# Kernel tuning notes

Measured on AMD Instinct MI355X. Metric: run time of the kernel, lower is better.

Reference implementation:

```python
import jax, jax.numpy as jnp
import numpy as np

LEAKY_SLOPE = 0.2
NEG_INF = -9e15
LN_EPS = 1e-5


def conv1x1(x, W, b):
    # x: [B, Cin, N, L], W: [Cout, Cin], b: [Cout] -> [B, Cout, N, L]
    return jnp.einsum('bcnl,oc->bonl', x, W) + b[None, :, None, None]


def gat_layer(h, mask, W, a, concat):
    # h: [B, L, N, Fin], mask: [N, N] bool, W: [Fin, Fout], a: [2*Fout, 1]
    Wh = h @ W                                   # [B, L, N, Fout]
    F_out = W.shape[1]
    Wh1 = Wh @ a[:F_out]                         # [B, L, N, 1]
    Wh2 = Wh @ a[F_out:]                         # [B, L, N, 1]
    e = jax.nn.leaky_relu(Wh1 + jnp.swapaxes(Wh2, -1, -2), LEAKY_SLOPE)  # [B,L,N,N]
    att = jnp.where(mask, e, NEG_INF)
    att = jax.nn.softmax(att, axis=-1)
    h_prime = att @ Wh                           # [B, L, N, Fout]
    return jax.nn.elu(h_prime) if concat else h_prime


def custom_layernorm(x):
    # normalizes over dims (1, 2) as in the torch LayerNorm (affine disabled)
    m = x.mean(axis=(1, 2), keepdims=True)
    v = x.var(axis=(1, 2), keepdims=True)
    return (x - m) / jnp.sqrt(v + LN_EPS)


def setup_inputs() -> dict:
    key = jax.random.key(0)
    ks = jax.random.split(key, 16)
    B, C, N, L = 4, 256, 1024, 12
    s = 0.06  # ~xavier scale for 256-dim fans
    return {
        'x_in': jax.random.normal(ks[0], (B, C, N, L), dtype=jnp.float32),
        'D_Graph': jax.random.randint(ks[1], (N, N), 0, 2, dtype=jnp.int32),
        'nodevec1': jax.random.normal(ks[2], (N, 6), dtype=jnp.float32),
        'nodevec2': jax.random.normal(ks[3], (6, N), dtype=jnp.float32),
        'W_mlp': jax.random.normal(ks[4], (C, 2 * C), dtype=jnp.float32) * 0.04,
        'b_mlp': jnp.zeros((C,), dtype=jnp.float32),
        'W_g0': jax.random.normal(ks[5], (C, C), dtype=jnp.float32) * s,
        'a_g0': jax.random.normal(ks[6], (2 * C, 1), dtype=jnp.float32) * s,
        'W_go': jax.random.normal(ks[7], (C, C), dtype=jnp.float32) * s,
        'a_go': jax.random.normal(ks[8], (2 * C, 1), dtype=jnp.float32) * s,
        'Wg1': jax.random.normal(ks[9], (C, C), dtype=jnp.float32) * s,
        'bg1': jnp.zeros((C,), dtype=jnp.float32),
        'Wg2': jax.random.normal(ks[10], (C, C), dtype=jnp.float32) * s,
        'bg2': jnp.zeros((C,), dtype=jnp.float32),
        'Wg3': jax.random.normal(ks[11], (C, C), dtype=jnp.float32) * s,
        'bg3': jnp.zeros((C,), dtype=jnp.float32),
        'alpha': jnp.float32(-5.0),
        'weight': jnp.ones((C, N, 1), dtype=jnp.float32),
        'bias': jnp.zeros((C, N, 1), dtype=jnp.float32),
    }


def reference(x_in, D_Graph, nodevec1, nodevec2, W_mlp, b_mlp, W_g0, a_g0,
              W_go, a_go, Wg1, bg1, Wg2, bg2, Wg3, bg3, alpha, weight, bias):
    # --- adaptive-adjacency GCN branch (support_len=1, order=1) ---
    adp = jax.nn.softmax(jax.nn.relu(nodevec1 @ nodevec2), axis=1)  # [N, N]
    x1 = jnp.einsum('bcvl,wv->bcwl', x_in, adp)
    h = jnp.concatenate([x_in, x1], axis=1)                         # [B, 2C, N, L]
    x_gcn = conv1x1(h, W_mlp, b_mlp)                                # [B, C, N, L]

    # --- dense adjacency-masked GAT branch (nheads=1, order=1) ---
    mask = D_Graph > 0
    ht = jnp.transpose(x_in, (0, 3, 2, 1))                          # [B, L, N, C]
    g = gat_layer(ht, mask, W_g0, a_g0, concat=True)
    g = jax.nn.elu(gat_layer(g, mask, W_go, a_go, concat=False))
    x_gat = jnp.transpose(g, (0, 3, 2, 1))                          # [B, C, N, L]

    # --- fuse, residual, norm, GLU, affine ---
    a_s = jax.nn.sigmoid(alpha)
    x = a_s * x_gat + (1.0 - a_s) * x_gcn + x_in
    x = custom_layernorm(x)
    g1 = conv1x1(x, Wg1, bg1)
    g2 = conv1x1(x, Wg2, bg2)
    glu_out = conv1x1(g1 * jax.nn.sigmoid(g2), Wg3, bg3)
    x = glu_out + x
    x = x * weight[None] + bias[None] + x
    x = custom_layernorm(x)
    return x
```

## Files before the change

kernel.cpp:

```cpp
#include <hip/hip_runtime.h>
#include <math.h>

#define DI __device__ __forceinline__
#define AS1 __attribute__((address_space(1)))
#define AS3 __attribute__((address_space(3)))

static constexpr int  B_ = 4, C_ = 256, N_ = 1024, L_ = 12, BL_ = 48;
static constexpr long SLAB = (long)N_ * C_;
static constexpr long TOT  = (long)BL_ * SLAB;

typedef __attribute__((ext_vector_type(8))) short bf16x8;
typedef __attribute__((ext_vector_type(4))) float f32x4;

DI float b2f(uint hw) { return __builtin_bit_cast(float, (hw & 0xffffu) << 16); }
DI ushort f2b(float f) {
    uint u = __builtin_bit_cast(uint, f);
    u += 0x7FFFu + ((u >> 16) & 1u);
    return (ushort)(u >> 16);
}

DI void gload16(const void* g, void* l) {
    __builtin_amdgcn_global_load_lds((AS1 uint*)g, (AS3 uint*)l, 16, 0, 0);
}

DI float block_sum256(float v, float* sc) {
    #pragma unroll
    for (int o = 32; o > 0; o >>= 1) v += __shfl_xor(v, o, 64);
    int wid = threadIdx.x >> 6;
    __syncthreads();
    if ((threadIdx.x & 63) == 0) sc[wid] = v;
    __syncthreads();
    return sc[0] + sc[1] + sc[2] + sc[3];
}
DI float block_max256(float v, float* sc) {
    #pragma unroll
    for (int o = 32; o > 0; o >>= 1) v = fmaxf(v, __shfl_xor(v, o, 64));
    int wid = threadIdx.x >> 6;
    __syncthreads();
    if ((threadIdx.x & 63) == 0) sc[wid] = v;
    __syncthreads();
    return fmaxf(fmaxf(sc[0], sc[1]), fmaxf(sc[2], sc[3]));
}

__global__ __launch_bounds__(256) void k_adp(const float* __restrict__ nv1,
                                             const float* __restrict__ nv2,
                                             ushort* __restrict__ adp) {
    __shared__ float r[6];
    __shared__ float sc[4];
    int row = blockIdx.x, tid = threadIdx.x;
    if (tid < 6) r[tid] = nv1[row * 6 + tid];
    __syncthreads();
    float e[4];
    #pragma unroll
    for (int q = 0; q < 4; q++) {
        int j = tid + q * 256;
        float s = 0.f;
        #pragma unroll
        for (int k = 0; k < 6; k++) s += r[k] * nv2[k * 1024 + j];
        e[q] = s > 0.f ? s : 0.f;
    }
    float m = fmaxf(fmaxf(e[0], e[1]), fmaxf(e[2], e[3]));
    m = block_max256(m, sc);
    float ps = 0.f;
    #pragma unroll
    for (int q = 0; q < 4; q++) { e[q] = __expf(e[q] - m); ps += e[q]; }
    ps = block_sum256(ps, sc);
    float rinv = 1.f / ps;
    #pragma unroll
    for (int q = 0; q < 4; q++) adp[(long)row * 1024 + tid + q * 256] = f2b(e[q] * rinv);
}

__global__ __launch_bounds__(256) void k_tin(const float* __restrict__ x,
                                             ushort* __restrict__ xb,
                                             float* __restrict__ xf) {
    __shared__ float t[64][65];
    int nl0 = blockIdx.x * 64, c0 = blockIdx.y * 64, b = blockIdx.z;
    int lx = threadIdx.x & 63, ly = threadIdx.x >> 6;
    #pragma unroll
    for (int i = 0; i < 16; i++) {
        int c = c0 + ly + i * 4;
        t[ly + i * 4][lx] = x[(long)(b * 256 + c) * 12288 + nl0 + lx];
    }
    __syncthreads();
    #pragma unroll
    for (int i = 0; i < 16; i++) {
        int nl = nl0 + ly + i * 4;
        int n = nl / 12, l = nl % 12;
        long idx = ((long)(b * 12 + l) * 1024 + n) * 256 + c0 + lx;
        float v = t[lx][ly + i * 4];
        xb[idx] = f2b(v);
        xf[idx] = v;
    }
}

__global__ __launch_bounds__(256) void k_xtt(const ushort* __restrict__ X,
                                             ushort* __restrict__ XT) {
    __shared__ ushort t[64][68];
    int bl = blockIdx.z;
    int n0 = blockIdx.x * 64, c0 = blockIdx.y * 64;
    int lx = threadIdx.x & 63, ly = threadIdx.x >> 6;
    const ushort* Xp = X + (long)bl * SLAB;
    #pragma unroll
    for (int i = 0; i < 16; i++)
        t[ly + i * 4][lx] = Xp[(long)(n0 + ly + i * 4) * 256 + c0 + lx];
    __syncthreads();
    ushort* Tp = XT + (long)bl * SLAB;
    #pragma unroll
    for (int i = 0; i < 16; i++)
        Tp[(long)(c0 + ly + i * 4) * 1024 + n0 + lx] = t[lx][ly + i * 4];
}

__global__ __launch_bounds__(256) void k_wt2(const float* __restrict__ S0, ushort* __restrict__ D0,
                                             const float* __restrict__ S1, ushort* __restrict__ D1) {
    __shared__ float t[64][65];
    const float* S = blockIdx.z ? S1 : S0;
    ushort* D = blockIdx.z ? D1 : D0;
    int c0 = blockIdx.x * 64, o0 = blockIdx.y * 64;
    int lx = threadIdx.x & 63, ly = threadIdx.x >> 6;
    #pragma unroll
    for (int i = 0; i < 16; i++)
        t[ly + i * 4][lx] = S[(long)(c0 + ly + i * 4) * 256 + o0 + lx];
    __syncthreads();
    #pragma unroll
    for (int i = 0; i < 16; i++)
        D[(long)(o0 + ly + i * 4) * 256 + c0 + lx] = f2b(t[lx][ly + i * 4]);
}

__global__ __launch_bounds__(256) void k_wconv(const float* __restrict__ S, ushort* __restrict__ D) {
    long i = (long)blockIdx.x * 256 + threadIdx.x;
    D[i] = f2b(S[i]);
}

__global__ __launch_bounds__(256) void k_wgi(const float* __restrict__ W1, const float* __restrict__ b1,
                                             const float* __restrict__ W2, const float* __restrict__ b2,
                                             ushort* __restrict__ WGI, float* __restrict__ BI) {
    int n = blockIdx.x, p = n >> 5, q = n & 31;
    const float* src = (q < 16) ? W1 + (long)(p * 16 + q) * 256
                                : W2 + (long)(p * 16 + q - 16) * 256;
    WGI[(long)n * 256 + threadIdx.x] = f2b(src[threadIdx.x]);
    if (threadIdx.x == 0) BI[n] = (q < 16) ? b1[p * 16 + q] : b2[p * 16 + q - 16];
}

__global__ __launch_bounds__(256) void k_va(const float* __restrict__ W, const float* __restrict__ a,
                                            float* __restrict__ va) {
    __shared__ float sc[4];
    int c = blockIdx.x, t = threadIdx.x;
    float w = W[(long)c * 256 + t];
    float s1 = block_sum256(w * a[t], sc);
    float s2 = block_sum256(w * a[256 + t], sc);
    if (t == 0) { va[c] = s1; va[256 + c] = s2; }
}

__global__ __launch_bounds__(256) void k_wtprep(const float* __restrict__ w,
                                                const float* __restrict__ b,
                                                float* __restrict__ wt,
                                                float* __restrict__ bt) {
    int n = blockIdx.x, c = threadIdx.x;
    wt[(long)n * 256 + c] = w[(long)c * 1024 + n] + 1.f;
    bt[(long)n * 256 + c] = b[(long)c * 1024 + n];
}

__global__ __launch_bounds__(256) void k_maskpack(const int* __restrict__ dg,
                                                  uint* __restrict__ maskw) {
    int w = blockIdx.x * 256 + threadIdx.x;
    int row = w >> 5, wo = w & 31;
    uint m = 0;
    #pragma unroll
    for (int b = 0; b < 32; b++)
        m |= (dg[(long)row * 1024 + wo * 32 + b] > 0 ? 1u : 0u) << b;
    maskw[w] = m;
}

template<int NPAIR, int GLU>
__global__ __launch_bounds__(256) void k_bgemm(
    const ushort* __restrict__ A0, long sA0,
    const ushort* __restrict__ A1, long sA1,
    int lda, int K0, int KK,
    const ushort* __restrict__ Bt, long sBt,
    const float* __restrict__ bias,
    float* __restrict__ Cf, ushort* __restrict__ Cb, long sC,
    const float* __restrict__ biasi) {
    __shared__ ushort As[128 * 32];
    __shared__ ushort Bs[128 * 32];
    const int tid = threadIdx.x;
    const int bl = blockIdx.z;
    const int m0 = blockIdx.x * 128, n0 = blockIdx.y * 128;
    const int N = gridDim.y * 128;
    const int lane = tid & 63, w = tid >> 6;
    const int wm = (w >> 1) * 64, wn = (w & 1) * 64;
    const int sr = tid >> 2, sk = (tid & 3) * 8;
    const int fr = lane & 15, fk = (lane >> 4) * 8;
    f32x4 acc[4][4] = {};
    const ushort* Ab0 = A0 + (long)bl * sA0;
    const ushort* Ab1 = (NPAIR == 2) ? A1 + (long)bl * sA1 : nullptr;
    const ushort* Bb = Bt + (long)bl * sBt;
    for (int k0 = 0; k0 < KK; k0 += 32) {
        const ushort* Asrc = Ab0; int kl = k0;
        if (NPAIR == 2 && k0 >= K0) { Asrc = Ab1; kl = k0 - K0; }
        __syncthreads();
        gload16(&Asrc[(long)(m0 + sr) * lda + kl + sk],      &As[sr * 32 + sk]);
        gload16(&Asrc[(long)(m0 + sr + 64) * lda + kl + sk], &As[(sr + 64) * 32 + sk]);
        gload16(&Bb[(long)(n0 + sr) * KK + k0 + sk],         &Bs[sr * 32 + sk]);
        gload16(&Bb[(long)(n0 + sr + 64) * KK + k0 + sk],    &Bs[(sr + 64) * 32 + sk]);
        __syncthreads();
        bf16x8 af[4], bg[4];
        #pragma unroll
        for (int i = 0; i < 4; i++) {
            af[i] = *(const bf16x8*)&As[(wm + i * 16 + fr) * 32 + fk];
            bg[i] = *(const bf16x8*)&Bs[(wn + i * 16 + fr) * 32 + fk];
        }
        #pragma unroll
        for (int i = 0; i < 4; i++)
            #pragma unroll
            for (int j = 0; j < 4; j++)
                acc[i][j] = __builtin_amdgcn_mfma_f32_16x16x32_bf16(af[i], bg[j], acc[i][j], 0, 0, 0);
    }
    const int cn = lane & 15, rb = (lane >> 4) * 4;
    if (GLU) {
        #pragma unroll
        for (int nt = 0; nt < 4; nt += 2) {
            int n1 = n0 + wn + nt * 16 + cn;
            int hcol = ((n1 >> 5) << 4) + cn;
            float b1 = biasi[n1], b2 = biasi[n1 + 16];
            #pragma unroll
            for (int i = 0; i < 4; i++) {
                #pragma unroll
                for (int r = 0; r < 4; r++) {
                    int m = m0 + wm + i * 16 + rb + r;
                    float g1 = acc[i][nt][r] + b1;
                    float g2 = acc[i][nt + 1][r] + b2;
                    float h = g1 / (1.f + __expf(-g2));
                    Cb[(long)bl * sC + (long)m * 256 + hcol] = f2b(h);
                }
            }
        }
    } else {
        #pragma unroll
        for (int j = 0; j < 4; j++) {
            int n = n0 + wn + j * 16 + cn;
            float bv = bias ? bias[n] : 0.f;
            #pragma unroll
            for (int i = 0; i < 4; i++) {
                #pragma unroll
                for (int r = 0; r < 4; r++) {
                    int m = m0 + wm + i * 16 + rb + r;
                    float v = acc[i][j][r] + bv;
                    long idx = (long)bl * sC + (long)m * N + n;
                    if (Cf) Cf[idx] = v;
                    if (Cb) Cb[idx] = f2b(v);
                }
            }
        }
    }
}

__global__ __launch_bounds__(256) void k_dots(const ushort* __restrict__ X,
                                              const float* __restrict__ va,
                                              float* __restrict__ o1,
                                              float* __restrict__ o2) {
    int wid = threadIdx.x >> 6, lane = threadIdx.x & 63;
    long row = (long)blockIdx.x * 4 + wid;
    uint2 xv = *(const uint2*)(X + row * 256 + lane * 4);
    float x0 = b2f(xv.x), x1 = b2f(xv.x >> 16), x2 = b2f(xv.y), x3 = b2f(xv.y >> 16);
    float4 v1 = *(const float4*)&va[lane * 4];
    float4 v2 = *(const float4*)&va[256 + lane * 4];
    float s1 = x0 * v1.x + x1 * v1.y + x2 * v1.z + x3 * v1.w;
    float s2 = x0 * v2.x + x1 * v2.y + x2 * v2.z + x3 * v2.w;
    #pragma unroll
    for (int o = 32; o > 0; o >>= 1) { s1 += __shfl_xor(s1, o, 64); s2 += __shfl_xor(s2, o, 64); }
    if (lane == 0) { o1[row] = s1; o2[row] = s2; }
}

DI float attn_p(float w1, float w2, uint bit, float mr) {
    float e = w1 + w2;
    e = e > 0.f ? e : 0.2f * e;
    float p = __expf(e - mr);
    return bit ? p : 0.f;
}

__global__ __launch_bounds__(256) void k_attn_mf(
    const ushort* __restrict__ WhT,
    const float* __restrict__ w1v, const float* __restrict__ w2v,
    const uint* __restrict__ maskw,
    ushort* __restrict__ outB) {
    __shared__ ushort P2[32 * 64 * 8];
    __shared__ float w2s[1024];
    __shared__ float w1s[64];
    __shared__ uint msk[64 * 33];
    __shared__ float pmax[4][64];
    __shared__ float psum[4][64];
    __shared__ float mrow[64];
    __shared__ float ssum[64];
    __shared__ float rsv[64];
    int d = blockIdx.x;
    int lidx = (d & 7) * 96 + (d >> 3);
    int bl = lidx >> 4;
    int i0 = (lidx & 15) * 64;
    int tid = threadIdx.x;
    #pragma unroll
    for (int q = 0; q < 4; q++) w2s[tid + q * 256] = w2v[(long)bl * 1024 + tid + q * 256];
    if (tid < 64) w1s[tid] = w1v[(long)bl * 1024 + i0 + tid];
    {
        const uint4* gm = (const uint4*)(maskw + (long)i0 * 32);
        uint4 ma = gm[tid * 2], mb = gm[tid * 2 + 1];
        int r0 = tid >> 2, w0 = (tid & 3) * 8;
        uint* mp = &msk[r0 * 33 + w0];
        mp[0] = ma.x; mp[1] = ma.y; mp[2] = ma.z; mp[3] = ma.w;
        mp[4] = mb.x; mp[5] = mb.y; mp[6] = mb.z; mp[7] = mb.w;
    }
    __syncthreads();
    const int row = tid & 63, jt = tid >> 6;
    float mloc = -1e30f;
    #pragma unroll
    for (int wq = 0; wq < 8; wq++) {
        uint mw = msk[row * 33 + jt * 8 + wq];
        int jb = jt * 256 + wq * 32;
        #pragma unroll
        for (int b = 0; b < 32; b++)
            mloc = fmaxf(mloc, ((mw >> b) & 1) ? w2s[jb + b] : -1e30f);
    }
    pmax[jt][row] = mloc;
    __syncthreads();
    if (tid < 64) {
        float m = fmaxf(fmaxf(pmax[0][tid], pmax[1][tid]), fmaxf(pmax[2][tid], pmax[3][tid]));
        float e = w1s[tid] + m;
        mrow[tid] = (e > 0.f) ? e : 0.2f * e;
        ssum[tid] = 0.f;
    }
    __syncthreads();
    const int lane = tid & 63, w = tid >> 6;
    const int wn = w * 64;
    const int fr = lane & 15, fk8 = (lane >> 4) * 8;
    f32x4 acc[4][4] = {};
    const ushort* bp = WhT + (long)bl * SLAB;
    const float w1r = w1s[row];
    const float mr = mrow[row];
    #pragma unroll 1
    for (int jc = 0; jc < 4; jc++) {
        int j0 = jc * 256;
        bf16x8 bgbuf[2][4];
        #pragma unroll
        for (int nt = 0; nt < 4; nt++)
            bgbuf[0][nt] = *(const bf16x8*)&bp[(long)(wn + nt * 16 + fr) * 1024 + j0 + fk8];
        uint mw0 = msk[row * 33 + jc * 8 + jt * 2];
        uint mw1 = msk[row * 33 + jc * 8 + jt * 2 + 1];
        float sloc = 0.f;
        #pragma unroll
        for (int u = 0; u < 8; u++) {
            uint mg = ((u & 4) ? mw1 : mw0) >> ((u & 3) * 8);
            int jb = j0 + jt * 64 + u * 8;
            float p0 = attn_p(w1r, w2s[jb + 0], mg & 1, mr);
            float p1 = attn_p(w1r, w2s[jb + 1], (mg >> 1) & 1, mr);
            float p2 = attn_p(w1r, w2s[jb + 2], (mg >> 2) & 1, mr);
            float p3 = attn_p(w1r, w2s[jb + 3], (mg >> 3) & 1, mr);
            float p4 = attn_p(w1r, w2s[jb + 4], (mg >> 4) & 1, mr);
            float p5 = attn_p(w1r, w2s[jb + 5], (mg >> 5) & 1, mr);
            float p6 = attn_p(w1r, w2s[jb + 6], (mg >> 6) & 1, mr);
            float p7 = attn_p(w1r, w2s[jb + 7], (mg >> 7) & 1, mr);
            sloc += p0 + p1 + p2 + p3 + p4 + p5 + p6 + p7;
            uint4 pv;
            pv.x = (uint)f2b(p0) | ((uint)f2b(p1) << 16);
            pv.y = (uint)f2b(p2) | ((uint)f2b(p3) << 16);
            pv.z = (uint)f2b(p4) | ((uint)f2b(p5) << 16);
            pv.w = (uint)f2b(p6) | ((uint)f2b(p7) << 16);
            int kq = jt * 8 + u;
            *(uint4*)((char*)P2 + (kq * 64 + row) * 16) = pv;
        }
        psum[jt][row] = sloc;
        __syncthreads();
        if (tid < 64)
            ssum[tid] += psum[0][tid] + psum[1][tid] + psum[2][tid] + psum[3][tid];
        #pragma unroll
        for (int ks = 0; ks < 8; ks++) {
            if (ks < 7) {
                int kb = (ks + 1) * 32 + fk8;
                #pragma unroll
                for (int nt = 0; nt < 4; nt++)
                    bgbuf[(ks + 1) & 1][nt] =
                        *(const bf16x8*)&bp[(long)(wn + nt * 16 + fr) * 1024 + j0 + kb];
            }
            int kq = ks * 4 + (lane >> 4);
            bf16x8 af[4];
            #pragma unroll
            for (int mt = 0; mt < 4; mt++)
                af[mt] = *(const bf16x8*)((char*)P2 + (kq * 64 + mt * 16 + fr) * 16);
            #pragma unroll
            for (int mt = 0; mt < 4; mt++)
                #pragma unroll
                for (int nt = 0; nt < 4; nt++)
                    acc[mt][nt] = __builtin_amdgcn_mfma_f32_16x16x32_bf16(
                        af[mt], bgbuf[ks & 1][nt], acc[mt][nt], 0, 0, 0);
        }
        __syncthreads();
    }
    if (tid < 64) rsv[tid] = 1.f / ssum[tid];
    __syncthreads();
    #pragma unroll
    for (int mt = 0; mt < 4; mt++) {
        #pragma unroll
        for (int r = 0; r < 4; r++) {
            int i = mt * 16 + (lane >> 4) * 4 + r;
            float sc = rsv[i];
            #pragma unroll
            for (int nt = 0; nt < 4; nt++) {
                int c = wn + nt * 16 + fr;
                float v = acc[mt][nt][r] * sc;
                v = (v > 0.f) ? v : __expf(v) - 1.f;
                outB[(long)bl * SLAB + (long)(i0 + i) * 256 + c] = f2b(v);
            }
        }
    }
}

__global__ __launch_bounds__(256) void k_fuse_ln(const ushort* __restrict__ gat,
                                                 const float4* __restrict__ gcn,
                                                 const float4* __restrict__ xf,
                                                 const float* __restrict__ alpha,
                                                 float4* __restrict__ o,
                                                 float2* __restrict__ part) {
    __shared__ float sc[4];
    int bl = blockIdx.y;
    long i = (long)bl * 65536 + blockIdx.x * 256 + threadIdx.x;
    float as = 1.f / (1.f + __expf(-alpha[0]));
    float bs = 1.f - as;
    uint2 hv = ((const uint2*)gat)[i];
    float4 g = gcn[i], x = xf[i];
    float4 v = make_float4(as * b2f(hv.x) + bs * g.x + x.x,
                           as * b2f(hv.x >> 16) + bs * g.y + x.y,
                           as * b2f(hv.y) + bs * g.z + x.z,
                           as * b2f(hv.y >> 16) + bs * g.w + x.w);
    o[i] = v;
    float s = v.x + v.y + v.z + v.w;
    float q = v.x * v.x + v.y * v.y + v.z * v.z + v.w * v.w;
    s = block_sum256(s, sc);
    q = block_sum256(q, sc);
    if (threadIdx.x == 0) part[bl * 256 + blockIdx.x] = make_float2(s, q);
}

__global__ __launch_bounds__(256) void k_stats256(const float2* __restrict__ part,
                                                  float2* __restrict__ stats) {
    __shared__ float sc[4];
    int bl = blockIdx.x;
    float2 v = part[bl * 256 + threadIdx.x];
    float s = block_sum256(v.x, sc);
    float q = block_sum256(v.y, sc);
    if (threadIdx.x == 0) {
        float mean = s / (float)SLAB;
        float var = q / (float)SLAB - mean * mean;
        stats[bl] = make_float2(mean, 1.f / sqrtf(var + 1e-5f));
    }
}

__global__ __launch_bounds__(256) void k_ln_apply(const float4* __restrict__ x,
                                                  const float2* __restrict__ stats,
                                                  float4* __restrict__ o,
                                                  ushort* __restrict__ ob) {
    long i = (long)blockIdx.x * 256 + threadIdx.x;
    int bl = (int)(i >> 16);
    float2 st = stats[bl];
    float4 v = x[i];
    float o0 = (v.x - st.x) * st.y, o1 = (v.y - st.x) * st.y;
    float o2 = (v.z - st.x) * st.y, o3 = (v.w - st.x) * st.y;
    o[i] = make_float4(o0, o1, o2, o3);
    uint2 ow;
    ow.x = (uint)f2b(o0) | ((uint)f2b(o1) << 16);
    ow.y = (uint)f2b(o2) | ((uint)f2b(o3) << 16);
    ((uint2*)ob)[i] = ow;
}

__global__ __launch_bounds__(256) void k_finpre_ln(const float4* __restrict__ glu,
                                                   const float4* __restrict__ xn,
                                                   const float4* __restrict__ wt,
                                                   const float4* __restrict__ bt,
                                                   float4* __restrict__ o,
                                                   float2* __restrict__ part) {
    __shared__ float sc[4];
    int bl = blockIdx.y;
    long i = (long)bl * 65536 + blockIdx.x * 256 + threadIdx.x;
    long wi = i & 65535;
    float4 g = glu[i], x = xn[i], w = wt[wi], b = bt[wi];
    float4 v = make_float4((g.x + x.x) * w.x + b.x, (g.y + x.y) * w.y + b.y,
                           (g.z + x.z) * w.z + b.z, (g.w + x.w) * w.w + b.w);
    o[i] = v;
    float s = v.x + v.y + v.z + v.w;
    float q = v.x * v.x + v.y * v.y + v.z * v.z + v.w * v.w;
    s = block_sum256(s, sc);
    q = block_sum256(q, sc);
    if (threadIdx.x == 0) part[bl * 256 + blockIdx.x] = make_float2(s, q);
}

__global__ __launch_bounds__(256) void k_out(const float* __restrict__ x,
                                             const float2* __restrict__ stats,
                                             float* __restrict__ out) {
    int n = blockIdx.x, b = blockIdx.y, c = threadIdx.x;
    float v[12];
    #pragma unroll
    for (int l = 0; l < 12; l++) {
        float2 st = stats[b * 12 + l];
        float t = x[(long)(b * 12 + l) * SLAB + (long)n * 256 + c];
        v[l] = (t - st.x) * st.y;
    }
    float4* op = (float4*)(out + ((long)(b * 256 + c) * 1024 + n) * 12);
    op[0] = make_float4(v[0], v[1], v[2], v[3]);
    op[1] = make_float4(v[4], v[5], v[6], v[7]);
    op[2] = make_float4(v[8], v[9], v[10], v[11]);
}

extern "C" void kernel_launch(void* const* d_in, const int* in_sizes, int n_in,
                              void* d_out, int out_size, void* d_ws, size_t ws_size,
                              hipStream_t stream) {
    (void)in_sizes; (void)n_in; (void)out_size; (void)ws_size;
    const float* x_in = (const float*)d_in[0];
    const int*   dg   = (const int*)d_in[1];
    const float* nv1  = (const float*)d_in[2];
    const float* nv2  = (const float*)d_in[3];
    const float* Wmlp = (const float*)d_in[4];
    const float* bmlp = (const float*)d_in[5];
    const float* Wg0  = (const float*)d_in[6];
    const float* ag0  = (const float*)d_in[7];
    const float* Wgo  = (const float*)d_in[8];
    const float* ago  = (const float*)d_in[9];
    const float* Wg1  = (const float*)d_in[10];
    const float* bg1  = (const float*)d_in[11];
    const float* Wg2  = (const float*)d_in[12];
    const float* bg2  = (const float*)d_in[13];
    const float* Wg3  = (const float*)d_in[14];
    const float* bg3  = (const float*)d_in[15];
    const float* alpha = (const float*)d_in[16];
    const float* wgt  = (const float*)d_in[17];
    const float* bia  = (const float*)d_in[18];
    float* out = (float*)d_out;

    float* XTf = (float*)d_ws;
    float* Bf  = XTf + TOT;
    ushort* U1 = (ushort*)(Bf + TOT);
    ushort* U2 = U1 + TOT;
    float* Af  = (float*)U1;
    ushort* U3 = U2 + TOT;
    ushort* U4 = U3 + TOT;
    ushort* ADPB = U4 + TOT;
    ushort* WMLPB = ADPB + (long)1024 * 1024;
    ushort* WG0T = WMLPB + 131072;
    ushort* WGOT = WG0T + 65536;
    ushort* WGIB = WGOT + 65536;
    ushort* WG3B = WGIB + 131072;
    float* BIASI = (float*)(WG3B + 65536);
    float* VA = BIASI + 512;
    float* W1V = VA + 1024;
    float* W2V = W1V + 49152;
    uint* MASKW = (uint*)(W2V + 49152);
    float2* PART = (float2*)(MASKW + 32768);
    float2* STATS = PART + 48 * 256;
    float* WT = (float*)(STATS + 48);
    float* BT2 = WT + SLAB;

    dim3 blk(256);
    k_wt2<<<dim3(4, 4, 2), blk, 0, stream>>>(Wg0, WG0T, Wgo, WGOT);
    k_wconv<<<512, blk, 0, stream>>>(Wmlp, WMLPB);
    k_wconv<<<256, blk, 0, stream>>>(Wg3, WG3B);
    k_wgi<<<512, blk, 0, stream>>>(Wg1, bg1, Wg2, bg2, WGIB, BIASI);
    k_va<<<256, blk, 0, stream>>>(Wg0, ag0, VA);
    k_va<<<256, blk, 0, stream>>>(Wgo, ago, VA + 512);
    k_wtprep<<<1024, blk, 0, stream>>>(wgt, bia, WT, BT2);
    k_adp<<<1024, blk, 0, stream>>>(nv1, nv2, ADPB);
    k_maskpack<<<128, blk, 0, stream>>>(dg, MASKW);
    k_tin<<<dim3(192, 4, 4), blk, 0, stream>>>(x_in, U1, XTf);
    k_xtt<<<dim3(16, 4, 48), blk, 0, stream>>>(U1, U2);
    k_bgemm<1, 0><<<dim3(8, 2, 48), blk, 0, stream>>>(ADPB, 0, nullptr, 0, 1024, 0, 1024,
                                                      U2, SLAB, nullptr, nullptr, U3, SLAB, nullptr);
    k_bgemm<2, 0><<<dim3(8, 2, 48), blk, 0, stream>>>(U1, SLAB, U3, SLAB, 256, 256, 512,
                                                      WMLPB, 0, bmlp, Bf, nullptr, SLAB, nullptr);
    k_dots<<<12288, blk, 0, stream>>>(U1, VA, W1V, W2V);
    k_bgemm<1, 0><<<dim3(2, 8, 48), blk, 0, stream>>>(WG0T, 0, nullptr, 0, 256, 0, 256,
                                                      U1, SLAB, nullptr, nullptr, U4, SLAB, nullptr);
    k_attn_mf<<<768, blk, 0, stream>>>(U4, W1V, W2V, MASKW, U2);
    k_dots<<<12288, blk, 0, stream>>>(U2, VA + 512, W1V, W2V);
    k_bgemm<1, 0><<<dim3(2, 8, 48), blk, 0, stream>>>(WGOT, 0, nullptr, 0, 256, 0, 256,
                                                      U2, SLAB, nullptr, nullptr, U4, SLAB, nullptr);
    k_attn_mf<<<768, blk, 0, stream>>>(U4, W1V, W2V, MASKW, U3);
    k_fuse_ln<<<dim3(256, 48), blk, 0, stream>>>(U3, (const float4*)Bf, (const float4*)XTf,
                                                 alpha, (float4*)Af, PART);
    k_stats256<<<48, blk, 0, stream>>>(PART, STATS);
    k_ln_apply<<<12288, blk, 0, stream>>>((const float4*)Af, STATS, (float4*)Bf, U3);
    k_bgemm<1, 1><<<dim3(8, 4, 48), blk, 0, stream>>>(U3, SLAB, nullptr, 0, 256, 0, 256,
                                                      WGIB, 0, nullptr, nullptr, U4, SLAB, BIASI);
    k_bgemm<1, 0><<<dim3(8, 2, 48), blk, 0, stream>>>(U4, SLAB, nullptr, 0, 256, 0, 256,
                                                      WG3B, 0, bg3, XTf, nullptr, SLAB, nullptr);
    k_finpre_ln<<<dim3(256, 48), blk, 0, stream>>>((const float4*)XTf, (const float4*)Bf,
                                                   (const float4*)WT, (const float4*)BT2,
                                                   (float4*)Af, PART);
    k_stats256<<<48, blk, 0, stream>>>(PART, STATS);
    k_out<<<dim3(1024, 4), blk, 0, stream>>>(Af, STATS, out);
}
```

Before: 569.4 us.

## Use unmasked per-slab w2 max as softmax shift, drop masked max pass

The attention kernel no longer computes a masked per-row max over 1024 columns. A small new kernel takes the unmasked max of w2 per slab, and each row's shift is leaky_relu(w1 + max w2), which is still an upper bound so the exponentials stay stable. Row sums are kept in registers and reduced once at the end instead of after every chunk. The software double-buffering of B fragments is replaced by plain per-step loads, and bf16 packing switches to the HIP intrinsic. The bound is looser than the true masked max, which risks small sums or underflow if masked-out entries dominate, and it adds one launch per layer.

```diff
diff --git a/kernel.cpp b/kernel.cpp
--- a/kernel.cpp
+++ b/kernel.cpp
@@ -1,4 +1,5 @@
 #include <hip/hip_runtime.h>
+#include <hip/hip_bf16.h>
 #include <math.h>
 
 #define DI __device__ __forceinline__
@@ -17,6 +18,12 @@
     uint u = __builtin_bit_cast(uint, f);
     u += 0x7FFFu + ((u >> 16) & 1u);
     return (ushort)(u >> 16);
+}
+DI uint pack2(float a, float b) {
+    __hip_bfloat162 h = __float22bfloat162_rn(make_float2(a, b));
+    uint r;
+    __builtin_memcpy(&r, &h, 4);
+    return r;
 }
 
 DI void gload16(const void* g, void* l) {
@@ -271,26 +278,27 @@
     if (lane == 0) { o1[row] = s1; o2[row] = s2; }
 }
 
-DI float attn_p(float w1, float w2, uint bit, float mr) {
-    float e = w1 + w2;
-    e = e > 0.f ? e : 0.2f * e;
-    float p = __expf(e - mr);
-    return bit ? p : 0.f;
+__global__ __launch_bounds__(256) void k_w2max(const float* __restrict__ w2v,
+                                               float* __restrict__ w2m) {
+    __shared__ float sc[4];
+    int bl = blockIdx.x;
+    float4 v = *(const float4*)&w2v[(long)bl * 1024 + threadIdx.x * 4];
+    float m = fmaxf(fmaxf(v.x, v.y), fmaxf(v.z, v.w));
+    m = block_max256(m, sc);
+    if (threadIdx.x == 0) w2m[bl] = m;
 }
 
 __global__ __launch_bounds__(256) void k_attn_mf(
     const ushort* __restrict__ WhT,
     const float* __restrict__ w1v, const float* __restrict__ w2v,
+    const float* __restrict__ w2m,
     const uint* __restrict__ maskw,
     ushort* __restrict__ outB) {
     __shared__ ushort P2[32 * 64 * 8];
     __shared__ float w2s[1024];
     __shared__ float w1s[64];
     __shared__ uint msk[64 * 33];
-    __shared__ float pmax[4][64];
     __shared__ float psum[4][64];
-    __shared__ float mrow[64];
-    __shared__ float ssum[64];
     __shared__ float rsv[64];
     int d = blockIdx.x;
     int lidx = (d & 7) * 96 + (d >> 3);
@@ -310,77 +318,49 @@
     }
     __syncthreads();
     const int row = tid & 63, jt = tid >> 6;
-    float mloc = -1e30f;
-    #pragma unroll
-    for (int wq = 0; wq < 8; wq++) {
-        uint mw = msk[row * 33 + jt * 8 + wq];
-        int jb = jt * 256 + wq * 32;
-        #pragma unroll
-        for (int b = 0; b < 32; b++)
-            mloc = fmaxf(mloc, ((mw >> b) & 1) ? w2s[jb + b] : -1e30f);
-    }
-    pmax[jt][row] = mloc;
-    __syncthreads();
-    if (tid < 64) {
-        float m = fmaxf(fmaxf(pmax[0][tid], pmax[1][tid]), fmaxf(pmax[2][tid], pmax[3][tid]));
-        float e = w1s[tid] + m;
-        mrow[tid] = (e > 0.f) ? e : 0.2f * e;
-        ssum[tid] = 0.f;
-    }
-    __syncthreads();
+    const float w1r = w1s[row];
+    float e0 = w1r + w2m[bl];
+    const float mr = (e0 > 0.f) ? e0 : 0.2f * e0;
+    float sloc = 0.f;
     const int lane = tid & 63, w = tid >> 6;
     const int wn = w * 64;
     const int fr = lane & 15, fk8 = (lane >> 4) * 8;
     f32x4 acc[4][4] = {};
     const ushort* bp = WhT + (long)bl * SLAB;
-    const float w1r = w1s[row];
-    const float mr = mrow[row];
     #pragma unroll 1
     for (int jc = 0; jc < 4; jc++) {
         int j0 = jc * 256;
-        bf16x8 bgbuf[2][4];
-        #pragma unroll
-        for (int nt = 0; nt < 4; nt++)
-            bgbuf[0][nt] = *(const bf16x8*)&bp[(long)(wn + nt * 16 + fr) * 1024 + j0 + fk8];
         uint mw0 = msk[row * 33 + jc * 8 + jt * 2];
         uint mw1 = msk[row * 33 + jc * 8 + jt * 2 + 1];
-        float sloc = 0.f;
         #pragma unroll
         for (int u = 0; u < 8; u++) {
             uint mg = ((u & 4) ? mw1 : mw0) >> ((u & 3) * 8);
             int jb = j0 + jt * 64 + u * 8;
-            float p0 = attn_p(w1r, w2s[jb + 0], mg & 1, mr);
-            float p1 = attn_p(w1r, w2s[jb + 1], (mg >> 1) & 1, mr);
-            float p2 = attn_p(w1r, w2s[jb + 2], (mg >> 2) & 1, mr);
-            float p3 = attn_p(w1r, w2s[jb + 3], (mg >> 3) & 1, mr);
-            float p4 = attn_p(w1r, w2s[jb + 4], (mg >> 4) & 1, mr);
-            float p5 = attn_p(w1r, w2s[jb + 5], (mg >> 5) & 1, mr);
-            float p6 = attn_p(w1r, w2s[jb + 6], (mg >> 6) & 1, mr);
-            float p7 = attn_p(w1r, w2s[jb + 7], (mg >> 7) & 1, mr);
-            sloc += p0 + p1 + p2 + p3 + p4 + p5 + p6 + p7;
+            float p[8];
+            #pragma unroll
+            for (int t = 0; t < 8; t++) {
+                float e = w1r + w2s[jb + t];
+                e = (e > 0.f) ? e : 0.2f * e;
+                float pp = __expf(e - mr);
+                p[t] = ((mg >> t) & 1) ? pp : 0.f;
+                sloc += p[t];
+            }
             uint4 pv;
-            pv.x = (uint)f2b(p0) | ((uint)f2b(p1) << 16);
-            pv.y = (uint)f2b(p2) | ((uint)f2b(p3) << 16);
-            pv.z = (uint)f2b(p4) | ((uint)f2b(p5) << 16);
-            pv.w = (uint)f2b(p6) | ((uint)f2b(p7) << 16);
-            int kq = jt * 8 + u;
-            *(uint4*)((char*)P2 + (kq * 64 + row) * 16) = pv;
+            pv.x = pack2(p[0], p[1]);
+            pv.y = pack2(p[2], p[3]);
+            pv.z = pack2(p[4], p[5]);
+            pv.w = pack2(p[6], p[7]);
+            *(uint4*)((char*)P2 + ((jt * 8 + u) * 64 + row) * 16) = pv;
         }
-        psum[jt][row] = sloc;
         __syncthreads();
-        if (tid < 64)
-            ssum[tid] += psum[0][tid] + psum[1][tid] + psum[2][tid] + psum[3][tid];
         #pragma unroll
         for (int ks = 0; ks < 8; ks++) {
-            if (ks < 7) {
-                int kb = (ks + 1) * 32 + fk8;
-                #pragma unroll
-                for (int nt = 0; nt < 4; nt++)
-                    bgbuf[(ks + 1) & 1][nt] =
-                        *(const bf16x8*)&bp[(long)(wn + nt * 16 + fr) * 1024 + j0 + kb];
-            }
+            int kb = ks * 32 + fk8;
+            bf16x8 bg[4], af[4];
+            #pragma unroll
+            for (int nt = 0; nt < 4; nt++)
+                bg[nt] = *(const bf16x8*)&bp[(long)(wn + nt * 16 + fr) * 1024 + j0 + kb];
             int kq = ks * 4 + (lane >> 4);
-            bf16x8 af[4];
             #pragma unroll
             for (int mt = 0; mt < 4; mt++)
                 af[mt] = *(const bf16x8*)((char*)P2 + (kq * 64 + mt * 16 + fr) * 16);
@@ -389,11 +369,14 @@
                 #pragma unroll
                 for (int nt = 0; nt < 4; nt++)
                     acc[mt][nt] = __builtin_amdgcn_mfma_f32_16x16x32_bf16(
-                        af[mt], bgbuf[ks & 1][nt], acc[mt][nt], 0, 0, 0);
+                        af[mt], bg[nt], acc[mt][nt], 0, 0, 0);
         }
         __syncthreads();
     }
-    if (tid < 64) rsv[tid] = 1.f / ssum[tid];
+    psum[jt][row] = sloc;
+    __syncthreads();
+    if (tid < 64)
+        rsv[tid] = 1.f / (psum[0][tid] + psum[1][tid] + psum[2][tid] + psum[3][tid]);
     __syncthreads();
     #pragma unroll
     for (int mt = 0; mt < 4; mt++) {
@@ -463,8 +446,8 @@
     float o2 = (v.z - st.x) * st.y, o3 = (v.w - st.x) * st.y;
     o[i] = make_float4(o0, o1, o2, o3);
     uint2 ow;
-    ow.x = (uint)f2b(o0) | ((uint)f2b(o1) << 16);
-    ow.y = (uint)f2b(o2) | ((uint)f2b(o3) << 16);
+    ow.x = pack2(o0, o1);
+    ow.y = pack2(o2, o3);
     ((uint2*)ob)[i] = ow;
 }
 
@@ -548,7 +531,8 @@
     float* VA = BIASI + 512;
     float* W1V = VA + 1024;
     float* W2V = W1V + 49152;
-    uint* MASKW = (uint*)(W2V + 49152);
+    float* W2M = W2V + 49152;
+    uint* MASKW = (uint*)(W2M + 64);
     float2* PART = (float2*)(MASKW + 32768);
     float2* STATS = PART + 48 * 256;
     float* WT = (float*)(STATS + 48);
@@ -571,13 +555,15 @@
     k_bgemm<2, 0><<<dim3(8, 2, 48), blk, 0, stream>>>(U1, SLAB, U3, SLAB, 256, 256, 512,
                                                       WMLPB, 0, bmlp, Bf, nullptr, SLAB, nullptr);
     k_dots<<<12288, blk, 0, stream>>>(U1, VA, W1V, W2V);
+    k_w2max<<<48, blk, 0, stream>>>(W2V, W2M);
     k_bgemm<1, 0><<<dim3(2, 8, 48), blk, 0, stream>>>(WG0T, 0, nullptr, 0, 256, 0, 256,
                                                       U1, SLAB, nullptr, nullptr, U4, SLAB, nullptr);
-    k_attn_mf<<<768, blk, 0, stream>>>(U4, W1V, W2V, MASKW, U2);
+    k_attn_mf<<<768, blk, 0, stream>>>(U4, W1V, W2V, W2M, MASKW, U2);
     k_dots<<<12288, blk, 0, stream>>>(U2, VA + 512, W1V, W2V);
+    k_w2max<<<48, blk, 0, stream>>>(W2V, W2M);
     k_bgemm<1, 0><<<dim3(2, 8, 48), blk, 0, stream>>>(WGOT, 0, nullptr, 0, 256, 0, 256,
                                                       U2, SLAB, nullptr, nullptr, U4, SLAB, nullptr);
-    k_attn_mf<<<768, blk, 0, stream>>>(U4, W1V, W2V, MASKW, U3);
+    k_attn_mf<<<768, blk, 0, stream>>>(U4, W1V, W2V, W2M, MASKW, U3);
     k_fuse_ln<<<dim3(256, 48), blk, 0, stream>>>(U3, (const float4*)Bf, (const float4*)XTf,
                                                  alpha, (float4*)Af, PART);
     k_stats256<<<48, blk, 0, stream>>>(PART, STATS);
```

After: 511.4 us. 10.2% less time.
